# Optimization experiments

Measured on AMD Instinct MI355X. Metric: run time of the kernel, lower is better.

## Reference

```python
import jax, jax.numpy as jnp
import numpy as np

B, S, D = 4, 2048, 1024
INV_SCALE = 32.0  # sqrt(D)


def setup_inputs() -> dict:
    key = jax.random.key(0)
    ks = jax.random.split(key, 7)
    std = 1.0 / np.sqrt(D)
    return {
        "x1": jax.random.normal(ks[0], (B, S, D), dtype=jnp.float32),
        "Wq": jax.random.normal(ks[1], (D, D), dtype=jnp.float32) * std,
        "bq": jax.random.normal(ks[2], (D,), dtype=jnp.float32) * std,
        "Wk": jax.random.normal(ks[3], (D, D), dtype=jnp.float32) * std,
        "bk": jax.random.normal(ks[4], (D,), dtype=jnp.float32) * std,
        "Wv": jax.random.normal(ks[5], (D, D), dtype=jnp.float32) * std,
        "bv": jax.random.normal(ks[6], (D,), dtype=jnp.float32) * std,
    }


def reference(x1, Wq, bq, Wk, bk, Wv, bv):
    # Linear projections (torch Linear: y = x @ W^T + b)
    q = jnp.einsum("bsd,ed->bse", x1, Wq) + bq
    k = jnp.einsum("bsd,ed->bse", x1, Wk) + bk
    v = jnp.einsum("bsd,ed->bse", x1, Wv) + bv
    # Attention: QK^T / inv_scale -> softmax -> (dropout is identity in eval) -> @V
    scores = jnp.einsum("bqd,bkd->bqk", q, k) / INV_SCALE
    attn = jax.nn.softmax(scores, axis=-1)
    out = jnp.einsum("bqk,bkd->bqd", attn, v)
    return out
```

## Files before the change

kernel.cpp:

```cpp
#include <hip/hip_runtime.h>
#include <cstdint>
#include <cstddef>

using bf16 = __bf16;
typedef float f32x4 __attribute__((ext_vector_type(4)));
typedef __bf16 bf16x8v __attribute__((ext_vector_type(8)));
typedef __bf16 bf16x4v __attribute__((ext_vector_type(4)));

#define NX   8388608
#define NW   1048576
#define SB   2048
#define DD   1024

__device__ __forceinline__ void gload_lds16(const bf16* g, bf16* l) {
    __builtin_amdgcn_global_load_lds(
        (const __attribute__((address_space(1))) void*)(g),
        (__attribute__((address_space(3))) void*)(l), 16, 0, 0);
}

__global__ __launch_bounds__(256)
void convert_kernel(const float* __restrict__ x1,
                    const float* __restrict__ Wq, const float* __restrict__ Wk,
                    const float* __restrict__ Wv,
                    const float* __restrict__ bq, const float* __restrict__ bk,
                    const float* __restrict__ bv,
                    bf16* __restrict__ xb, bf16* __restrict__ wb,
                    float* __restrict__ biases)
{
    const int NX4 = NX / 4;
    const int NW4 = NW / 4;
    const int NMAT = NX4 + 3 * NW4;
    const int total = NMAT + 768;
    for (int i = blockIdx.x * 256 + threadIdx.x; i < total; i += gridDim.x * 256) {
        if (i < NMAT) {
            const float* src; bf16* dst; int j;
            if (i < NX4) { src = x1; dst = xb; j = i; }
            else {
                int w = (i - NX4) / NW4;
                j = (i - NX4) - w * NW4;
                src = (w == 0) ? Wq : (w == 1) ? Wk : Wv;
                dst = wb + (size_t)w * NW;
            }
            float4 f = ((const float4*)src)[j];
            bf16x4v o;
            o[0] = (bf16)f.x; o[1] = (bf16)f.y; o[2] = (bf16)f.z; o[3] = (bf16)f.w;
            ((bf16x4v*)dst)[j] = o;
        } else {
            int j = i - NMAT;
            const float* src = (j < 256) ? bq : (j < 512) ? bk : bv;
            ((float4*)biases)[j] = ((const float4*)src)[j & 255];
        }
    }
}

template<int V, typename OutT>
__global__ __launch_bounds__(256)
void gemm_bt(const bf16* __restrict__ A, const bf16* __restrict__ B,
             OutT* __restrict__ C, bf16* __restrict__ vT,
             const float* __restrict__ bias, float* __restrict__ pRow,
             int N, int K,
             long sAz, long sBz, long sCz, float scale)
{
    __shared__ bf16 lA[2][128 * 64];
    __shared__ bf16 lB[2][128 * 64];
    __shared__ float inv[128];
    const int z = blockIdx.z;
    A += (size_t)z * sAz;
    B += (size_t)z * sBz;
    C += (size_t)z * sCz;
    if constexpr (V == 1 || V == 2) pRow += (size_t)z * (SB * 32);

    const int gx = gridDim.x;
    const int nwg = gx * gridDim.y;
    const int orig = (int)blockIdx.y * gx + (int)blockIdx.x;
    const int q8 = nwg >> 3;
    const int tile = (orig & 7) * q8 + (orig >> 3);
    const int bx = tile % gx;
    const int by = tile / gx;

    const int n0 = bx * 128;
    const int m0 = by * 128;
    const int t = threadIdx.x;
    const int lane = t & 63;
    const int wid = t >> 6;
    const int wr = wid >> 1, wc = wid & 1;

    if constexpr (V == 2) {
        if (t < 128) {
            const float4* pr = (const float4*)&pRow[(size_t)(m0 + t) * 32];
            float s = 0.f;
            #pragma unroll
            for (int j = 0; j < 8; ++j) {
                float4 f = pr[j];
                s += f.x + f.y + f.z + f.w;
            }
            inv[t] = 1.0f / s;
        }
        __syncthreads();
    }

    f32x4 acc[4][4];
    #pragma unroll
    for (int m = 0; m < 4; ++m)
        #pragma unroll
        for (int n = 0; n < 4; ++n) acc[m][n] = (f32x4){0.f, 0.f, 0.f, 0.f};

    auto stage = [&](int b, int k0) {
        #pragma unroll
        for (int l = 0; l < 4; ++l) {
            const int idx = l * 256 + t;
            const int row = idx >> 3;
            const int c   = idx & 7;
            const int gc  = c ^ (row & 7);
            gload_lds16(A + (size_t)(m0 + row) * K + k0 + gc * 8, &lA[b][idx * 8]);
            gload_lds16(B + (size_t)(n0 + row) * K + k0 + gc * 8, &lB[b][idx * 8]);
        }
    };

    const int NT = K >> 6;

    stage(0, 0);
    stage(1, 64);

    for (int tt = 0; tt < NT; ++tt) {
        const int cur = tt & 1;
        if (tt == NT - 1) asm volatile("s_waitcnt vmcnt(0)" ::: "memory");
        else              asm volatile("s_waitcnt vmcnt(8)" ::: "memory");
        __builtin_amdgcn_s_barrier();

        bf16x8v af[2][4], bfr[2][4];
        #pragma unroll
        for (int kk = 0; kk < 2; ++kk) {
            #pragma unroll
            for (int m = 0; m < 4; ++m) {
                const int row = wr * 64 + m * 16 + (lane & 15);
                const int ch  = (kk * 4 + (lane >> 4)) ^ (row & 7);
                af[kk][m] = *(const bf16x8v*)&lA[cur][row * 64 + ch * 8];
            }
            #pragma unroll
            for (int n = 0; n < 4; ++n) {
                const int row = wc * 64 + n * 16 + (lane & 15);
                const int ch  = (kk * 4 + (lane >> 4)) ^ (row & 7);
                bfr[kk][n] = *(const bf16x8v*)&lB[cur][row * 64 + ch * 8];
            }
        }
        asm volatile("s_waitcnt lgkmcnt(0)" ::: "memory");
        __builtin_amdgcn_sched_barrier(0);
        __builtin_amdgcn_s_barrier();

        if (tt + 2 < NT) stage(cur, (tt + 2) * 64);

        #pragma unroll
        for (int kk = 0; kk < 2; ++kk)
            #pragma unroll
            for (int m = 0; m < 4; ++m)
                #pragma unroll
                for (int n = 0; n < 4; ++n)
                    acc[m][n] = __builtin_amdgcn_mfma_f32_16x16x32_bf16(
                        af[kk][m], bfr[kk][n], acc[m][n], 0, 0, 0);
    }

    const int cif = lane & 15;
    const int rif = (lane >> 4) << 2;

    if constexpr (V == 1) {
        const float sc2 = scale * 1.4426950408889634f;
        const float sh2 = -8.656170245333781f;
        float rs[4][4];
        #pragma unroll
        for (int m = 0; m < 4; ++m)
            #pragma unroll
            for (int r = 0; r < 4; ++r) rs[m][r] = 0.f;

        #pragma unroll
        for (int m = 0; m < 4; ++m) {
            const int gm = m0 + wr * 64 + m * 16 + rif;
            #pragma unroll
            for (int n = 0; n < 4; ++n) {
                const int col = n0 + wc * 64 + n * 16 + cif;
                #pragma unroll
                for (int r = 0; r < 4; ++r) {
                    const float e = exp2f(fmaf(acc[m][n][r], sc2, sh2));
                    rs[m][r] += e;
                    C[(size_t)(gm + r) * N + col] = (OutT)e;
                }
            }
        }
        #pragma unroll
        for (int m = 0; m < 4; ++m)
            #pragma unroll
            for (int r = 0; r < 4; ++r) {
                #pragma unroll
                for (int msk = 1; msk < 16; msk <<= 1)
                    rs[m][r] += __shfl_xor(rs[m][r], msk);
            }
        if ((lane & 15) == 0) {
            const int slot = bx * 2 + wc;
            #pragma unroll
            for (int m = 0; m < 4; ++m) {
                const int gm = m0 + wr * 64 + m * 16 + rif;
                #pragma unroll
                for (int r = 0; r < 4; ++r)
                    pRow[(size_t)(gm + r) * 32 + slot] = rs[m][r];
            }
        }
    } else {
        #pragma unroll
        for (int m = 0; m < 4; ++m) {
            const int gm = m0 + wr * 64 + m * 16 + rif;
            #pragma unroll
            for (int n = 0; n < 4; ++n) {
                const int col = n0 + wc * 64 + n * 16 + cif;
                if constexpr (V == 0) {
                    const float bb = bias[col];
                    if (col < 1024) {
                        #pragma unroll
                        for (int r = 0; r < 4; ++r)
                            C[(size_t)(gm + r) * 1024 + col] = (OutT)(acc[m][n][r] + bb);
                    } else if (col < 2048) {
                        #pragma unroll
                        for (int r = 0; r < 4; ++r)
                            C[NX + (size_t)(gm + r) * 1024 + (col - 1024)] = (OutT)(acc[m][n][r] + bb);
                    } else {
                        const int batch = gm >> 11, s = gm & 2047, d = col - 2048;
                        bf16x4v pk;
                        #pragma unroll
                        for (int r = 0; r < 4; ++r) pk[r] = (bf16)(acc[m][n][r] + bb);
                        *(bf16x4v*)&vT[((size_t)batch << 21) + ((size_t)d << 11) + s] = pk;
                    }
                } else {
                    const int rloc = wr * 64 + m * 16 + rif;
                    #pragma unroll
                    for (int r = 0; r < 4; ++r)
                        C[(size_t)(gm + r) * N + col] = (OutT)(acc[m][n][r] * inv[rloc + r]);
                }
            }
        }
    }
}

extern "C" void kernel_launch(void* const* d_in, const int* in_sizes, int n_in,
                              void* d_out, int out_size, void* d_ws, size_t ws_size,
                              hipStream_t stream)
{
    const float* x1 = (const float*)d_in[0];
    const float* Wq = (const float*)d_in[1];
    const float* bq = (const float*)d_in[2];
    const float* Wk = (const float*)d_in[3];
    const float* bk = (const float*)d_in[4];
    const float* Wv = (const float*)d_in[5];
    const float* bv = (const float*)d_in[6];
    float* out = (float*)d_out;

    bf16* xb     = (bf16*)d_ws;
    bf16* wb     = xb + NX;
    bf16* qkb    = wb + 3 * NW;
    bf16* vTb    = qkb + 2 * (size_t)NX;
    bf16* scores = vTb + NX;
    float* biases = (float*)(scores + 4 * (size_t)SB * SB);
    float* partial = (float*)xb;

    convert_kernel<<<dim3(2048), dim3(256), 0, stream>>>(
        x1, Wq, Wk, Wv, bq, bk, bv, xb, wb, biases);

    gemm_bt<0, bf16><<<dim3(24, 64, 1), dim3(256), 0, stream>>>(
        xb, wb, qkb, vTb, biases, nullptr, 1024, 1024, 0L, 0L, 0L, 1.0f);

    gemm_bt<1, bf16><<<dim3(16, 16, 4), dim3(256), 0, stream>>>(
        qkb, qkb + NX, scores, nullptr, nullptr, partial, SB, DD,
        (long)(SB * DD), (long)(SB * DD), (long)(SB * SB), 1.0f / 32.0f);

    gemm_bt<2, float><<<dim3(8, 16, 4), dim3(256), 0, stream>>>(
        scores, vTb, out, nullptr, nullptr, partial, DD, SB,
        (long)(SB * SB), (long)(SB * DD), (long)(SB * DD), 1.0f);
}
```

Baseline: 162.3 us.

## Software-pipeline LDS fragment reads with MFMA using double register buffers

Restructures the GEMM main loop so the LDS fragment reads for the next K-tile are issued between the two MFMA halves of the current tile, using ping-pong register fragment sets and a loop unrolled by two. The MFMA blocks are also wrapped in s_setprio to favour matrix issue. The aim is to hide LDS read latency behind matrix math rather than stalling on lgkmcnt before every tile. In exchange it doubles fragment register use, which may lower occupancy, and the unroll-by-two assumes NT is even.

Measured after the change: 252.5 us. +55.6%, slower.

```diff
diff --git a/kernel.cpp b/kernel.cpp
--- a/kernel.cpp
+++ b/kernel.cpp
@@ -11,6 +11,8 @@
 #define NW   1048576
 #define SB   2048
 #define DD   1024
+
+#define VMCNT(n) asm volatile("s_waitcnt vmcnt(" #n ")" ::: "memory")
 
 __device__ __forceinline__ void gload_lds16(const bf16* g, bf16* l) {
     __builtin_amdgcn_global_load_lds(
@@ -84,6 +86,7 @@
     const int lane = t & 63;
     const int wid = t >> 6;
     const int wr = wid >> 1, wc = wid & 1;
+    const int rl = lane & 15, lg = lane >> 4;
 
     if constexpr (V == 2) {
         if (t < 128) {
@@ -119,49 +122,63 @@
 
     const int NT = K >> 6;
 
+#define READS(BUF, AF, BF) do {                                            \
+        _Pragma("unroll") for (int kk = 0; kk < 2; ++kk) {                 \
+            _Pragma("unroll") for (int m = 0; m < 4; ++m) {                \
+                const int row = wr * 64 + m * 16 + rl;                     \
+                const int ch  = (kk * 4 + lg) ^ (row & 7);                 \
+                AF[kk][m] = *(const bf16x8v*)&lA[BUF][row * 64 + ch * 8];  \
+            }                                                              \
+            _Pragma("unroll") for (int n = 0; n < 4; ++n) {                \
+                const int row = wc * 64 + n * 16 + rl;                     \
+                const int ch  = (kk * 4 + lg) ^ (row & 7);                 \
+                BF[kk][n] = *(const bf16x8v*)&lB[BUF][row * 64 + ch * 8];  \
+            }                                                              \
+        }                                                                  \
+    } while (0)
+
+#define MFMAH(KK, AF, BF) do {                                             \
+        __builtin_amdgcn_s_setprio(1);                                     \
+        _Pragma("unroll") for (int m = 0; m < 4; ++m)                      \
+            _Pragma("unroll") for (int n = 0; n < 4; ++n)                  \
+                acc[m][n] = __builtin_amdgcn_mfma_f32_16x16x32_bf16(       \
+                    AF[KK][m], BF[KK][n], acc[m][n], 0, 0, 0);             \
+        __builtin_amdgcn_s_setprio(0);                                     \
+    } while (0)
+
+#define ITER(TT, ACUR, BCUR, ANXT, BNXT) do {                              \
+        const int cur = (TT) & 1;                                          \
+        asm volatile("s_waitcnt lgkmcnt(0)" ::: "memory");                 \
+        __builtin_amdgcn_s_barrier();                                      \
+        if ((TT) + 2 < NT) stage(cur, ((TT) + 2) * 64);                    \
+        MFMAH(0, ACUR, BCUR);                                              \
+        if ((TT) + 1 < NT) {                                               \
+            if ((TT) + 2 < NT) { VMCNT(8); } else { VMCNT(0); }            \
+            __builtin_amdgcn_s_barrier();                                  \
+            READS(cur ^ 1, ANXT, BNXT);                                    \
+            __builtin_amdgcn_sched_barrier(0);                             \
+        }                                                                  \
+        MFMAH(1, ACUR, BCUR);                                              \
+    } while (0)
+
     stage(0, 0);
     stage(1, 64);
-
-    for (int tt = 0; tt < NT; ++tt) {
-        const int cur = tt & 1;
-        if (tt == NT - 1) asm volatile("s_waitcnt vmcnt(0)" ::: "memory");
-        else              asm volatile("s_waitcnt vmcnt(8)" ::: "memory");
-        __builtin_amdgcn_s_barrier();
-
-        bf16x8v af[2][4], bfr[2][4];
-        #pragma unroll
-        for (int kk = 0; kk < 2; ++kk) {
-            #pragma unroll
-            for (int m = 0; m < 4; ++m) {
-                const int row = wr * 64 + m * 16 + (lane & 15);
-                const int ch  = (kk * 4 + (lane >> 4)) ^ (row & 7);
-                af[kk][m] = *(const bf16x8v*)&lA[cur][row * 64 + ch * 8];
-            }
-            #pragma unroll
-            for (int n = 0; n < 4; ++n) {
-                const int row = wc * 64 + n * 16 + (lane & 15);
-                const int ch  = (kk * 4 + (lane >> 4)) ^ (row & 7);
-                bfr[kk][n] = *(const bf16x8v*)&lB[cur][row * 64 + ch * 8];
-            }
-        }
-        asm volatile("s_waitcnt lgkmcnt(0)" ::: "memory");
-        __builtin_amdgcn_sched_barrier(0);
-        __builtin_amdgcn_s_barrier();
-
-        if (tt + 2 < NT) stage(cur, (tt + 2) * 64);
-
-        #pragma unroll
-        for (int kk = 0; kk < 2; ++kk)
-            #pragma unroll
-            for (int m = 0; m < 4; ++m)
-                #pragma unroll
-                for (int n = 0; n < 4; ++n)
-                    acc[m][n] = __builtin_amdgcn_mfma_f32_16x16x32_bf16(
-                        af[kk][m], bfr[kk][n], acc[m][n], 0, 0, 0);
-    }
-
-    const int cif = lane & 15;
-    const int rif = (lane >> 4) << 2;
+    VMCNT(8);
+    __builtin_amdgcn_s_barrier();
+    bf16x8v afA[2][4], bfA[2][4], afB[2][4], bfB[2][4];
+    READS(0, afA, bfA);
+    __builtin_amdgcn_sched_barrier(0);
+
+    for (int tt = 0; tt < NT; tt += 2) {
+        ITER(tt,     afA, bfA, afB, bfB);
+        ITER(tt + 1, afB, bfB, afA, bfA);
+    }
+#undef READS
+#undef MFMAH
+#undef ITER
+
+    const int cif = rl;
+    const int rif = lg << 2;
 
     if constexpr (V == 1) {
         const float sc2 = scale * 1.4426950408889634f;
```
